# Optimization experiments

Measured on AMD Instinct MI355X. Metric: run time of the kernel, lower is better.

The kernel has to match this reference:

```python
import jax, jax.numpy as jnp
import numpy as np

B, K, D = 16384, 512, 256

def setup_inputs() -> dict:
    key = jax.random.key(0)
    kz, kc = jax.random.split(key)
    z = jax.random.normal(kz, (B, D), dtype=jnp.float32)
    # matches nn.Parameter(torch.randn(n_codes, d_dim) * 0.1)
    codebook = jax.random.normal(kc, (K, D), dtype=jnp.float32) * 0.1
    return {"z": z, "codebook": codebook}

def reference(z, codebook):
    """Eval-mode forward of SFDiVeQ: project each z onto the nearest line
    segment between consecutive codewords. Vectorizes the original Python
    loop over K-1 segments via GEMMs; returns (z_q, indices, lambdas, dists).
    """
    c_i = codebook[:-1]                    # (K-1, D) segment starts
    seg = codebook[1:] - c_i               # (K-1, D) segment vectors
    seg_len_sq = jnp.sum(seg * seg, axis=-1) + 1e-8        # (K-1,)

    # t = ((z - c_i) . seg) / |seg|^2, clamped to [0, 1]
    dot = z @ seg.T - jnp.sum(c_i * seg, axis=-1)          # (B, K-1) = (z - c_i).seg
    t = jnp.clip(dot / seg_len_sq, 0.0, 1.0)               # (B, K-1)

    # |z - c_i|^2 via expansion (avoids (B, K-1, D) intermediate)
    zz = jnp.sum(z * z, axis=-1, keepdims=True)            # (B, 1)
    cc = jnp.sum(c_i * c_i, axis=-1)                       # (K-1,)
    zc = z @ c_i.T                                         # (B, K-1)
    d0 = zz - 2.0 * zc + cc                                # (B, K-1)

    # |z - (c_i + t*seg)|^2 = |z - c_i|^2 - 2 t (z - c_i).seg + t^2 |seg|^2
    dist_sq = jnp.maximum(d0 - 2.0 * t * dot + t * t * seg_len_sq, 0.0)
    dists_all = jnp.sqrt(dist_sq)                          # (B, K-1)

    # running-min with strict '<' keeps first minimum -> argmin (first tie) matches
    idx = jnp.argmin(dists_all, axis=-1)                   # (B,) int
    rows = jnp.arange(z.shape[0])
    t_best = t[rows, idx]                                  # (B,) lambdas
    best_point = c_i[idx] + t_best[:, None] * seg[idx]     # (B, D) nearest = z_q (eval)
    dists = dists_all[rows, idx]                           # (B,)
    return best_point, idx, t_best, dists
```

## Files before the change

### kernel.cpp

```cpp
#include <hip/hip_runtime.h>
#include <math.h>

#define B_ROWS 16384
#define K_CB   512
#define D_DIM  256
#define NSEG   511
#define NG     4

#define WS_WBND 1536
#define WS_ZZ   50688
#define WS_CAND 67072

__global__ __launch_bounds__(256) void prologue_kernel(const float* __restrict__ z,
                                                       const float* __restrict__ cb,
                                                       float* __restrict__ sls,
                                                       float* __restrict__ cs,
                                                       float* __restrict__ cc,
                                                       float* __restrict__ wbnd,
                                                       float* __restrict__ zz) {
    int bid = blockIdx.x;
    int t = threadIdx.x;
    int lane = t & 63;
    if (bid < 128) {
        int j = bid * 4 + (t >> 6);
        if (j == NSEG) {
            if (lane == 0) { sls[NSEG] = 1e30f; cs[NSEG] = 0.f; cc[NSEG] = 0.f; }
            return;
        }
        float4 a = reinterpret_cast<const float4*>(cb + (size_t)j * D_DIM)[lane];
        float4 b = reinterpret_cast<const float4*>(cb + (size_t)(j + 1) * D_DIM)[lane];
        float sx = b.x - a.x, sy = b.y - a.y, sz = b.z - a.z, sw = b.w - a.w;
        float p0 = sx*sx + sy*sy + sz*sz + sw*sw;
        float p1 = a.x*sx + a.y*sy + a.z*sz + a.w*sw;
        float p2 = a.x*a.x + a.y*a.y + a.z*a.z + a.w*a.w;
        #pragma unroll
        for (int m = 32; m >= 1; m >>= 1) {
            p0 += __shfl_xor(p0, m);
            p1 += __shfl_xor(p1, m);
            p2 += __shfl_xor(p2, m);
        }
        if (lane == 0) { sls[j] = p0 + 1e-8f; cs[j] = p1; cc[j] = p2; }
    } else {
        int row = (bid - 128) * 4 + (t >> 6);
        float4 zv = reinterpret_cast<const float4*>(z + (size_t)row * D_DIM)[lane];
        float pz = zv.x*zv.x + zv.y*zv.y + zv.z*zv.z + zv.w*zv.w;
        #pragma unroll
        for (int m = 32; m >= 1; m >>= 1) pz += __shfl_xor(pz, m);
        if (lane == 0) zz[row] = pz;
        #pragma unroll
        for (int gi = 0; gi < 3; ++gi) {
            int col = 128 * (gi + 1);
            float4 cv = reinterpret_cast<const float4*>(cb + (size_t)col * D_DIM)[lane];
            float p = zv.x*cv.x + zv.y*cv.y + zv.z*cv.z + zv.w*cv.w;
            #pragma unroll
            for (int m = 32; m >= 1; m >>= 1) p += __shfl_xor(p, m);
            if (lane == 0) wbnd[(size_t)gi * B_ROWS + row] = p;
        }
    }
}

__global__ __launch_bounds__(256, 2) void main_kernel(const float* __restrict__ z,
                                                      const float* __restrict__ cb,
                                                      const float* __restrict__ sls_g,
                                                      const float* __restrict__ cs_g,
                                                      const float* __restrict__ cc_g,
                                                      const float* __restrict__ wbnd,
                                                      float4* __restrict__ cand) {
    __shared__ __align__(16) float zs[128][36];
    __shared__ __align__(16) float csh[128][36];
    __shared__ float sl_s[128], cs_s[128], cc_s[128];

    int t = threadIdx.x;
    int row0 = blockIdx.x * 128;
    int g = blockIdx.y;
    int col0 = g * 128;
    int tr = t >> 4;
    int tc = t & 15;
    int l = t & 63;

    if (t < 128) {
        sl_s[t] = sls_g[col0 + t];
        cs_s[t] = cs_g[col0 + t];
        cc_s[t] = cc_g[col0 + t];
    }

    float acc[8][8];
    #pragma unroll
    for (int r = 0; r < 8; ++r)
        #pragma unroll
        for (int c = 0; c < 8; ++c) acc[r][c] = 0.f;

    for (int kc = 0; kc < 8; ++kc) {
        int d0 = kc * 32;
        __syncthreads();
        #pragma unroll
        for (int i = 0; i < 4; ++i) {
            int f = i * 256 + t;
            int r = f >> 3;
            int kq = f & 7;
            float4 v = *reinterpret_cast<const float4*>(z + (size_t)(row0 + r) * D_DIM + d0 + kq * 4);
            *reinterpret_cast<float4*>(&zs[r][kq * 4]) = v;
            float4 w = *reinterpret_cast<const float4*>(cb + (size_t)(col0 + r) * D_DIM + d0 + kq * 4);
            *reinterpret_cast<float4*>(&csh[r][kq * 4]) = w;
        }
        __syncthreads();
        #pragma unroll
        for (int k4 = 0; k4 < 8; ++k4) {
            float4 za[8];
            #pragma unroll
            for (int r = 0; r < 8; ++r)
                za[r] = *reinterpret_cast<const float4*>(&zs[tr + 16 * r][k4 * 4]);
            #pragma unroll
            for (int c = 0; c < 8; ++c) {
                float4 cv = *reinterpret_cast<const float4*>(&csh[tc + 16 * c][k4 * 4]);
                #pragma unroll
                for (int r = 0; r < 8; ++r) {
                    acc[r][c] += za[r].x * cv.x;
                    acc[r][c] += za[r].y * cv.y;
                    acc[r][c] += za[r].z * cv.z;
                    acc[r][c] += za[r].w * cv.w;
                }
            }
        }
    }

    float wbv[8];
    #pragma unroll
    for (int r = 0; r < 8; ++r) wbv[r] = 0.f;
    if (g < 3 && tc == 15) {
        #pragma unroll
        for (int r = 0; r < 8; ++r)
            wbv[r] = wbnd[(size_t)g * B_ROWS + row0 + tr + 16 * r];
    }

    #pragma unroll
    for (int r = 0; r < 8; ++r) {
        int row = tr + 16 * r;
        float firstw[8];
        #pragma unroll
        for (int c = 1; c < 8; ++c) firstw[c] = __shfl(acc[r][c], l & 48);
        float bd = 1e38f; int bj = 0x3fffffff; float bt = 0.f;
        #pragma unroll
        for (int c = 0; c < 8; ++c) {
            float w0 = acc[r][c];
            float shA = __shfl(w0, l + 1);
            float w1 = (tc == 15) ? ((c < 7) ? firstw[c + 1] : wbv[r]) : shA;
            int jl = tc + 16 * c;
            int j = col0 + jl;
            float slsj = sl_s[jl], csj = cs_s[jl], ccj = cc_s[jl];
            float dot = w1 - w0 - csj;
            float tt = fminf(fmaxf(dot / slsj, 0.f), 1.f);
            float d2 = ccj - 2.f * w0 + tt * (tt * slsj - 2.f * dot);
            if (j < NSEG && d2 < bd) { bd = d2; bj = j; bt = tt; }
        }
        #pragma unroll
        for (int m = 1; m <= 8; m <<= 1) {
            float od = __shfl_xor(bd, m);
            int   oj = __shfl_xor(bj, m);
            float ot = __shfl_xor(bt, m);
            if (od < bd || (od == bd && oj < bj)) { bd = od; bj = oj; bt = ot; }
        }
        if (tc == 0)
            cand[(size_t)(row0 + row) * NG + g] = make_float4(bd, bt, (float)bj, 0.f);
    }
}

__global__ __launch_bounds__(256) void combine_kernel(const float4* __restrict__ cand,
                                                      const float* __restrict__ cb,
                                                      const float* __restrict__ zz,
                                                      float* __restrict__ out) {
    float* out_bp  = out;
    float* out_idx = out + (size_t)B_ROWS * D_DIM;
    float* out_t   = out_idx + B_ROWS;
    float* out_d   = out_t + B_ROWS;

    __shared__ float sj[8];
    __shared__ float st8[8];

    int t = threadIdx.x;
    int row0 = blockIdx.x * 8;
    if (t < 8) {
        int row = row0 + t;
        const float4* cp = cand + (size_t)row * NG;
        float4 c0 = cp[0], c1 = cp[1], c2 = cp[2], c3 = cp[3];
        float bd = c0.x, bt = c0.y, bj = c0.z;
        if (c1.x < bd) { bd = c1.x; bt = c1.y; bj = c1.z; }
        if (c2.x < bd) { bd = c2.x; bt = c2.y; bj = c2.z; }
        if (c3.x < bd) { bd = c3.x; bt = c3.y; bj = c3.z; }
        sj[t] = bj; st8[t] = bt;
        out_idx[row] = bj;
        out_t[row]   = bt;
        out_d[row]   = sqrtf(fmaxf(bd + zz[row], 0.f));
    }
    __syncthreads();

    int lane = t & 63, w = t >> 6;
    #pragma unroll
    for (int it = 0; it < 2; ++it) {
        int rl = it * 4 + w;
        int j = (int)sj[rl];
        float tt = st8[rl];
        float4 a = reinterpret_cast<const float4*>(cb + (size_t)j * D_DIM)[lane];
        float4 b = reinterpret_cast<const float4*>(cb + (size_t)(j + 1) * D_DIM)[lane];
        float4 bp = make_float4(a.x + tt * (b.x - a.x),
                                a.y + tt * (b.y - a.y),
                                a.z + tt * (b.z - a.z),
                                a.w + tt * (b.w - a.w));
        reinterpret_cast<float4*>(out_bp + (size_t)(row0 + rl) * D_DIM)[lane] = bp;
    }
}

extern "C" void kernel_launch(void* const* d_in, const int* in_sizes, int n_in,
                              void* d_out, int out_size, void* d_ws, size_t ws_size,
                              hipStream_t stream) {
    const float* z  = (const float*)d_in[0];
    const float* cb = (const float*)d_in[1];
    float* ws  = (float*)d_ws;
    float* sls  = ws;
    float* cs   = ws + 512;
    float* cc   = ws + 1024;
    float* wbnd = ws + WS_WBND;
    float* zz   = ws + WS_ZZ;
    float4* cand = (float4*)(ws + WS_CAND);
    float* out = (float*)d_out;

    prologue_kernel<<<128 + B_ROWS / 4, 256, 0, stream>>>(z, cb, sls, cs, cc, wbnd, zz);
    main_kernel<<<dim3(B_ROWS / 128, NG), 256, 0, stream>>>(z, cb, sls, cs, cc, wbnd, cand);
    combine_kernel<<<B_ROWS / 8, 256, 0, stream>>>(cand, cb, zz, out);
}
```

Measured before the change: 140.5 us.

## Load GEMM tiles with direct global-to-LDS copies into XOR-swizzled shared memory

```diff
diff --git a/kernel.cpp b/kernel.cpp
--- a/kernel.cpp
+++ b/kernel.cpp
@@ -1,11 +1,15 @@
 #include <hip/hip_runtime.h>
 #include <math.h>
+#include <stdint.h>
 
 #define B_ROWS 16384
 #define K_CB   512
 #define D_DIM  256
 #define NSEG   511
 #define NG     4
+
+#define AS1 __attribute__((address_space(1)))
+#define AS3 __attribute__((address_space(3)))
 
 #define WS_WBND 1536
 #define WS_ZZ   50688
@@ -59,15 +63,15 @@
     }
 }
 
-__global__ __launch_bounds__(256, 2) void main_kernel(const float* __restrict__ z,
-                                                      const float* __restrict__ cb,
-                                                      const float* __restrict__ sls_g,
-                                                      const float* __restrict__ cs_g,
-                                                      const float* __restrict__ cc_g,
-                                                      const float* __restrict__ wbnd,
-                                                      float4* __restrict__ cand) {
-    __shared__ __align__(16) float zs[128][36];
-    __shared__ __align__(16) float csh[128][36];
+__global__ __launch_bounds__(256) void main_kernel(const float* __restrict__ z,
+                                                   const float* __restrict__ cb,
+                                                   const float* __restrict__ sls_g,
+                                                   const float* __restrict__ cs_g,
+                                                   const float* __restrict__ cc_g,
+                                                   const float* __restrict__ wbnd,
+                                                   float4* __restrict__ cand) {
+    __shared__ __align__(16) float zs[128 * 64];
+    __shared__ __align__(16) float csh[128 * 64];
     __shared__ float sl_s[128], cs_s[128], cc_s[128];
 
     int t = threadIdx.x;
@@ -77,6 +81,7 @@
     int tr = t >> 4;
     int tc = t & 15;
     int l = t & 63;
+    int w = t >> 6;
 
     if (t < 128) {
         sl_s[t] = sls_g[col0 + t];
@@ -90,29 +95,37 @@
         #pragma unroll
         for (int c = 0; c < 8; ++c) acc[r][c] = 0.f;
 
-    for (int kc = 0; kc < 8; ++kc) {
-        int d0 = kc * 32;
+    for (int kc = 0; kc < 4; ++kc) {
+        int d0 = kc * 64;
         __syncthreads();
         #pragma unroll
-        for (int i = 0; i < 4; ++i) {
+        for (int i = 0; i < 8; ++i) {
             int f = i * 256 + t;
-            int r = f >> 3;
-            int kq = f & 7;
-            float4 v = *reinterpret_cast<const float4*>(z + (size_t)(row0 + r) * D_DIM + d0 + kq * 4);
-            *reinterpret_cast<float4*>(&zs[r][kq * 4]) = v;
-            float4 w = *reinterpret_cast<const float4*>(cb + (size_t)(col0 + r) * D_DIM + d0 + kq * 4);
-            *reinterpret_cast<float4*>(&csh[r][kq * 4]) = w;
+            int r = f >> 4;
+            int kq = f & 15;
+            int srcq = kq ^ (r & 15);
+            const float* gz = z + (size_t)(row0 + r) * D_DIM + d0 + srcq * 4;
+            float* lz = &zs[(size_t)(i * 256 + w * 64) * 4];
+            __builtin_amdgcn_global_load_lds((AS1 void*)(uintptr_t)gz,
+                                             (AS3 void*)(uintptr_t)lz, 16, 0, 0);
+            const float* gc = cb + (size_t)(col0 + r) * D_DIM + d0 + srcq * 4;
+            float* lc = &csh[(size_t)(i * 256 + w * 64) * 4];
+            __builtin_amdgcn_global_load_lds((AS1 void*)(uintptr_t)gc,
+                                             (AS3 void*)(uintptr_t)lc, 16, 0, 0);
         }
         __syncthreads();
         #pragma unroll
-        for (int k4 = 0; k4 < 8; ++k4) {
+        for (int k4 = 0; k4 < 16; ++k4) {
             float4 za[8];
             #pragma unroll
-            for (int r = 0; r < 8; ++r)
-                za[r] = *reinterpret_cast<const float4*>(&zs[tr + 16 * r][k4 * 4]);
+            for (int r = 0; r < 8; ++r) {
+                int row = tr + 16 * r;
+                za[r] = *reinterpret_cast<const float4*>(&zs[(size_t)(row * 16 + (k4 ^ tr)) * 4]);
+            }
             #pragma unroll
             for (int c = 0; c < 8; ++c) {
-                float4 cv = *reinterpret_cast<const float4*>(&csh[tc + 16 * c][k4 * 4]);
+                int row = tc + 16 * c;
+                float4 cv = *reinterpret_cast<const float4*>(&csh[(size_t)(row * 16 + (k4 ^ tc)) * 4]);
                 #pragma unroll
                 for (int r = 0; r < 8; ++r) {
                     acc[r][c] += za[r].x * cv.x;
```

New measurement: 194.2 us. 1.38x slower.
